# Performance work log

Measured on AMD Instinct MI355X. Metric: run time of the kernel, lower is better.

## Reference

```python
import jax, jax.numpy as jnp
import numpy as np

N = 50000      # nodes per graph batch (per side)
E = 600000     # edges per side
B = 4096       # number of graphs (drug pairs)
D = 128        # node_dim == hidden_dim
K = 128        # kge_dim
R = 86         # rel_total
L = 3          # n_iter
EPS = 1e-5


def setup_inputs() -> dict:
    key = jax.random.key(0)
    ks = jax.random.split(key, 16)
    inp = {}
    inp["x1"] = jax.random.normal(ks[0], (N, D), jnp.float32)
    inp["x2"] = jax.random.normal(ks[1], (N, D), jnp.float32)
    inp["edge_index1"] = jax.random.randint(ks[2], (2, E), 0, N)
    inp["edge_index2"] = jax.random.randint(ks[3], (2, E), 0, N)
    inp["batch1"] = jnp.sort(jax.random.randint(ks[4], (N,), 0, B))
    inp["batch2"] = jnp.sort(jax.random.randint(ks[5], (N,), 0, B))
    inp["rel"] = jax.random.randint(ks[6], (B,), 0, R)
    # SAGEConv params, stacked over L layers (all [D,D] since node_dim==hidden_dim)
    sc = 0.05
    inp["Wl"] = jax.random.normal(ks[7], (L, D, D), jnp.float32) * sc   # lin on aggregated neighbors (has bias)
    inp["bl"] = jnp.zeros((L, D), jnp.float32)
    inp["Wr"] = jax.random.normal(ks[8], (L, D, D), jnp.float32) * sc   # root (self) lin, no bias
    # BatchNorm (eval mode: running stats)
    inp["bn_gamma"] = jnp.ones((L, D), jnp.float32)
    inp["bn_beta"] = jnp.zeros((L, D), jnp.float32)
    inp["bn_mean"] = jnp.zeros((L, D), jnp.float32)
    inp["bn_var"] = jnp.ones((L, D), jnp.float32)
    # relation embedding + final MLP
    inp["kge"] = jax.random.normal(ks[9], (R, K), jnp.float32)
    inp["W1"] = jax.random.normal(ks[10], (2 * D + K, D), jnp.float32) * sc
    inp["b1"] = jnp.zeros((D,), jnp.float32)
    inp["W2"] = jax.random.normal(ks[11], (D, 1), jnp.float32) * sc
    inp["b2"] = jnp.zeros((1,), jnp.float32)
    return inp


def _gnn(x, edge_index, Wl, bl, Wr, g, b, m, v):
    src, dst = edge_index[0], edge_index[1]
    deg = jax.ops.segment_sum(jnp.ones((E,), x.dtype), dst, num_segments=N)
    deg = jnp.maximum(deg, 1.0)[:, None]
    for i in range(L):
        agg = jax.ops.segment_sum(x[src], dst, num_segments=N) / deg  # mean aggregation
        h = agg @ Wl[i] + bl[i] + x @ Wr[i]                           # SAGEConv
        h = (h - m[i]) * (g[i] / jnp.sqrt(v[i] + EPS)) + b[i]         # BN (eval)
        x = jax.nn.relu(h)                                            # dropout = identity (eval)
    return x


def reference(x1, edge_index1, batch1, x2, edge_index2, batch2, rel,
              Wl, bl, Wr, bn_gamma, bn_beta, bn_mean, bn_var,
              kge, W1, b1, W2, b2):
    h1 = _gnn(x1, edge_index1, Wl, bl, Wr, bn_gamma, bn_beta, bn_mean, bn_var)
    h2 = _gnn(x2, edge_index2, Wl, bl, Wr, bn_gamma, bn_beta, bn_mean, bn_var)
    p1 = jax.ops.segment_sum(h1, batch1, num_segments=B)  # global_add_pool
    p2 = jax.ops.segment_sum(h2, batch2, num_segments=B)
    r = kge[rel]                                          # [B, K]
    z = jnp.concatenate([p1, p2, r], axis=-1)             # [B, 2D+K]
    h = jax.nn.relu(z @ W1 + b1)
    out = h @ W2 + b2
    return out.reshape(-1)
```

## Files before the change

### kernel.cpp

```cpp
#include <hip/hip_runtime.h>

#define NN 50000
#define NE 600000
#define NB 4096
#define DD 128
#define EPSV 1e-5f
#define NBKT 196
#define NCHUNK 256
#define CHSZ ((NE + NCHUNK - 1) / NCHUNK)

typedef __bf16 bf16x8 __attribute__((ext_vector_type(8)));
typedef float f32x4 __attribute__((ext_vector_type(4)));

__device__ inline unsigned short f2bf(float f) {
    unsigned u = __float_as_uint(f);
    u = (u + 0x7FFFu + ((u >> 16) & 1u)) >> 16;
    return (unsigned short)u;
}
__device__ inline float bf2f(unsigned short h) {
    return __uint_as_float(((unsigned)h) << 16);
}

__global__ void k_cvt(const float* __restrict__ x1, const float* __restrict__ x2,
                      unsigned short* __restrict__ xh, unsigned short* __restrict__ xl) {
    int i = blockIdx.x * 256 + threadIdx.x;
    if (i >= 2 * NN * 32) return;
    const float* x = (i < NN * 32) ? x1 : x2;
    int j = (i < NN * 32) ? i : i - NN * 32;
    float4 v = ((const float4*)x)[j];
    ushort4 h, l;
    h.x = f2bf(v.x); l.x = f2bf(v.x - bf2f(h.x));
    h.y = f2bf(v.y); l.y = f2bf(v.y - bf2f(h.y));
    h.z = f2bf(v.z); l.z = f2bf(v.z - bf2f(h.z));
    h.w = f2bf(v.w); l.w = f2bf(v.w - bf2f(h.w));
    ((ushort4*)xh)[i] = h;
    ((ushort4*)xl)[i] = l;
}

__global__ void k_wcvt(const float* __restrict__ Wl, const float* __restrict__ Wr,
                       const float* __restrict__ W1, unsigned* __restrict__ wtp) {
    int t = blockIdx.x * 256 + threadIdx.x;
    if (t >= 3 * 128 * 256 + 128 * 384) return;
    float w;
    int idx;
    if (t < 3 * 128 * 256) {
        int k = t & 255;
        int n = (t >> 8) & 127;
        int l = t >> 15;
        w = (k < 128) ? Wl[l * 16384 + k * 128 + n] : Wr[l * 16384 + (k - 128) * 128 + n];
        idx = t;
    } else {
        int u = t - 3 * 128 * 256;
        int n = u / 384;
        int k = u - n * 384;
        w = W1[k * 128 + n];
        idx = t;
    }
    unsigned short h = f2bf(w);
    unsigned short l = f2bf(w - bf2f(h));
    wtp[idx] = ((unsigned)h << 16) | (unsigned)l;
}

__global__ void k_hist(const int* __restrict__ d0, const int* __restrict__ d1,
                       int* __restrict__ bcnt) {
    int side = (blockIdx.x >= NCHUNK) ? 1 : 0;
    int c = blockIdx.x - side * NCHUNK;
    const int* dst = side ? d1 : d0;
    int tid = threadIdx.x;
    __shared__ int h[NBKT];
    for (int i = tid; i < NBKT; i += 256) h[i] = 0;
    __syncthreads();
    int e0 = c * CHSZ, e1 = min(e0 + CHSZ, NE);
    for (int e = e0 + tid; e < e1; e += 256) atomicAdd(&h[dst[e] >> 8], 1);
    __syncthreads();
    int* bc = bcnt + ((size_t)side * NCHUNK + c) * NBKT;
    for (int i = tid; i < NBKT; i += 256) bc[i] = h[i];
}

__global__ void k_s1(int* __restrict__ bcnt, int* __restrict__ btot) {
    int side = (blockIdx.x >= NBKT) ? 1 : 0;
    int b = blockIdx.x - side * NBKT;
    int tid = threadIdx.x;
    int idx = ((size_t)side * NCHUNK + tid) * NBKT + b;
    int v = bcnt[idx];
    int lane = tid & 63, wv = tid >> 6;
    int x = v;
#pragma unroll
    for (int off = 1; off < 64; off <<= 1) {
        int y = __shfl_up(x, off, 64);
        if (lane >= off) x += y;
    }
    __shared__ int ws4[4];
    if (lane == 63) ws4[wv] = x;
    __syncthreads();
    int add = 0;
#pragma unroll
    for (int w = 0; w < 4; w++)
        if (w < wv) add += ws4[w];
    int incl = x + add;
    bcnt[idx] = incl - v;
    if (tid == 255) btot[side * NBKT + b] = incl;
}

__global__ void k_s2(const int* __restrict__ btot, int* __restrict__ bbase,
                     int* __restrict__ ptrC) {
    int side = blockIdx.x;
    int tid = threadIdx.x;
    int v = (tid < NBKT) ? btot[side * NBKT + tid] : 0;
    int lane = tid & 63, wv = tid >> 6;
    int x = v;
#pragma unroll
    for (int off = 1; off < 64; off <<= 1) {
        int y = __shfl_up(x, off, 64);
        if (lane >= off) x += y;
    }
    __shared__ int ws4[4];
    if (lane == 63) ws4[wv] = x;
    __syncthreads();
    int add = 0;
#pragma unroll
    for (int w = 0; w < 4; w++)
        if (w < wv) add += ws4[w];
    int incl = x + add;
    if (tid < NBKT) bbase[side * NBKT + tid] = incl - v;
    if (tid == 0 && side == 1) ptrC[2 * NN] = 2 * NE;
}

__global__ void k_part(const int* __restrict__ s0, const int* __restrict__ d0,
                       const int* __restrict__ s1, const int* __restrict__ d1,
                       const int* __restrict__ bcnt, const int* __restrict__ bbase,
                       int* __restrict__ part) {
    int side = (blockIdx.x >= NCHUNK) ? 1 : 0;
    int c = blockIdx.x - side * NCHUNK;
    const int* src = side ? s1 : s0;
    const int* dst = side ? d1 : d0;
    int tid = threadIdx.x;
    __shared__ int off[NBKT];
    const int* bc = bcnt + ((size_t)side * NCHUNK + c) * NBKT;
    for (int i = tid; i < NBKT; i += 256) off[i] = bbase[side * NBKT + i] + bc[i];
    __syncthreads();
    int e0 = c * CHSZ, e1 = min(e0 + CHSZ, NE);
    int* P = part + (size_t)side * NE;
    int soff = side * NN;
    for (int e = e0 + tid; e < e1; e += 256) {
        int d = dst[e];
        int pos = atomicAdd(&off[d >> 8], 1);
        P[pos] = ((src[e] + soff) << 8) | (d & 255);
    }
}

__global__ void k_csr(const int* __restrict__ part, const int* __restrict__ bbase,
                      int* __restrict__ ptrC, float* __restrict__ invdC,
                      int* __restrict__ csrC) {
    int side = (blockIdx.x >= NBKT) ? 1 : 0;
    int b = blockIdx.x - side * NBKT;
    int tid = threadIdx.x;
    const int* P = part + (size_t)side * NE;
    int base = bbase[side * NBKT + b];
    int endp = (b == NBKT - 1) ? NE : bbase[side * NBKT + b + 1];
    __shared__ int cnt[256];
    cnt[tid] = 0;
    __syncthreads();
    for (int e = base + tid; e < endp; e += 256) atomicAdd(&cnt[P[e] & 255], 1);
    __syncthreads();
    int v = cnt[tid];
    int lane = tid & 63, wv = tid >> 6;
    int x = v;
#pragma unroll
    for (int off = 1; off < 64; off <<= 1) {
        int y = __shfl_up(x, off, 64);
        if (lane >= off) x += y;
    }
    __shared__ int ws4[4];
    if (lane == 63) ws4[wv] = x;
    __syncthreads();
    int add = 0;
#pragma unroll
    for (int w = 0; w < 4; w++)
        if (w < wv) add += ws4[w];
    int excl = x + add - v;
    int node = (b << 8) + tid;
    if (node < NN) {
        ptrC[side * NN + node] = side * NE + base + excl;
        invdC[side * NN + node] = 1.0f / (float)(v > 1 ? v : 1);
    }
    __syncthreads();
    cnt[tid] = excl;
    __syncthreads();
    for (int e = base + tid; e < endp; e += 256) {
        int p = P[e];
        int pos = atomicAdd(&cnt[p & 255], 1);
        csrC[(size_t)side * NE + base + pos] = p >> 8;
    }
}

__global__ void k_gather(const unsigned short* __restrict__ xh, const int* __restrict__ ptr,
                         const int* __restrict__ csr, const float* __restrict__ invd,
                         unsigned short* __restrict__ aggH) {
    int wid = threadIdx.x >> 6;
    int lane = threadIdx.x & 63;
    int q = lane >> 4;
    int c = lane & 15;
    int n = blockIdx.x * 4 + wid;
    if (n >= 2 * NN) return;
    int beg = ptr[n], end = ptr[n + 1];
    float id = invd[n];
    float a[8];
#pragma unroll
    for (int k = 0; k < 8; k++) a[k] = 0.f;

    for (int base = beg; base < end; base += 64) {
        int cnt = min(end - base, 64);
        int idxv = csr[base + min(lane, cnt - 1)];
        for (int e0 = 0; e0 < cnt; e0 += 8) {
            int eA = e0 + q;
            int eB = e0 + 4 + q;
            int iA = __shfl(idxv, eA, 64);
            int iB = __shfl(idxv, eB, 64);
            float wA = (eA < cnt) ? 1.f : 0.f;
            float wB = (eB < cnt) ? 1.f : 0.f;
            uint4 vA = *(const uint4*)(xh + (((unsigned)iA << 7) + (c << 3)));
            uint4 vB = *(const uint4*)(xh + (((unsigned)iB << 7) + (c << 3)));
            a[0] += wA * __uint_as_float(vA.x << 16);
            a[1] += wA * __uint_as_float(vA.x & 0xffff0000u);
            a[2] += wA * __uint_as_float(vA.y << 16);
            a[3] += wA * __uint_as_float(vA.y & 0xffff0000u);
            a[4] += wA * __uint_as_float(vA.z << 16);
            a[5] += wA * __uint_as_float(vA.z & 0xffff0000u);
            a[6] += wA * __uint_as_float(vA.w << 16);
            a[7] += wA * __uint_as_float(vA.w & 0xffff0000u);
            a[0] += wB * __uint_as_float(vB.x << 16);
            a[1] += wB * __uint_as_float(vB.x & 0xffff0000u);
            a[2] += wB * __uint_as_float(vB.y << 16);
            a[3] += wB * __uint_as_float(vB.y & 0xffff0000u);
            a[4] += wB * __uint_as_float(vB.z << 16);
            a[5] += wB * __uint_as_float(vB.z & 0xffff0000u);
            a[6] += wB * __uint_as_float(vB.w << 16);
            a[7] += wB * __uint_as_float(vB.w & 0xffff0000u);
        }
    }
#pragma unroll
    for (int k = 0; k < 8; k++) {
        a[k] += __shfl_xor(a[k], 16, 64);
        a[k] += __shfl_xor(a[k], 32, 64);
    }
    if (q == 0) {
        unsigned short h0 = f2bf(a[0] * id), h1 = f2bf(a[1] * id);
        unsigned short h2 = f2bf(a[2] * id), h3 = f2bf(a[3] * id);
        unsigned short h4 = f2bf(a[4] * id), h5 = f2bf(a[5] * id);
        unsigned short h6 = f2bf(a[6] * id), h7 = f2bf(a[7] * id);
        uint4 o;
        o.x = (unsigned)h0 | ((unsigned)h1 << 16);
        o.y = (unsigned)h2 | ((unsigned)h3 << 16);
        o.z = (unsigned)h4 | ((unsigned)h5 << 16);
        o.w = (unsigned)h6 | ((unsigned)h7 << 16);
        *(uint4*)(aggH + (size_t)n * DD + c * 8) = o;
    }
}

__launch_bounds__(256)
__global__ void k_gemm(const unsigned short* __restrict__ AH,
                       const unsigned short* __restrict__ XH, const unsigned short* __restrict__ XL,
                       const unsigned* __restrict__ Wtp,
                       const float* __restrict__ bl, const float* __restrict__ g,
                       const float* __restrict__ be, const float* __restrict__ mn,
                       const float* __restrict__ vr,
                       unsigned short* __restrict__ OH, unsigned short* __restrict__ OL,
                       float* __restrict__ Of, int f32out) {
    __shared__ __align__(16) unsigned short sA[2][64 * 40];
    __shared__ __align__(16) unsigned short sW[2][64 * 40];
    int tid = threadIdx.x;
    int gx = blockIdx.x;
    int m0 = (gx >> 1) * 64;
    int n0 = (gx & 1) * 64;
    int lane = tid & 63;
    int w = tid >> 6;
    int fm = lane & 15, q = lane >> 4;
    int wr = (w & 1) * 32;
    int wn = (w >> 1) * 32;

    f32x4 acc[2][2];
#pragma unroll
    for (int i = 0; i < 2; i++)
#pragma unroll
        for (int j = 0; j < 2; j++) acc[i][j] = (f32x4){0.f, 0.f, 0.f, 0.f};

    for (int c = 0; c < 8; c++) {
        int isA = (c < 4);
        const unsigned short* SH = isA ? AH : XH;
        const unsigned short* SL = isA ? (const unsigned short*)0 : XL;
        int k0 = (c & 3) * 32;
        int k0W = c * 32;
        __syncthreads();
#pragma unroll
        for (int i = 0; i < 2; i++) {
            int u = tid + 256 * i;
            int row = u >> 3, seg = u & 7;
            int grow = m0 + row;
            size_t goff = (size_t)grow * DD + k0 + seg * 4;
            ushort4 hv = make_ushort4(0, 0, 0, 0);
            if (grow < 2 * NN) hv = *(const ushort4*)(SH + goff);
            *(ushort4*)&sA[0][row * 40 + seg * 4] = hv;
            if (!isA) {
                ushort4 lv = make_ushort4(0, 0, 0, 0);
                if (grow < 2 * NN) lv = *(const ushort4*)(SL + goff);
                *(ushort4*)&sA[1][row * 40 + seg * 4] = lv;
            }
        }
#pragma unroll
        for (int i = 0; i < 2; i++) {
            int u = tid + 256 * i;
            int row = u >> 3, seg = u & 7;
            uint4 val = *(const uint4*)(Wtp + (size_t)(n0 + row) * 256 + k0W + seg * 4);
            ushort4 hi, lo;
            hi.x = val.x >> 16; hi.y = val.y >> 16; hi.z = val.z >> 16; hi.w = val.w >> 16;
            lo.x = val.x & 0xFFFF; lo.y = val.y & 0xFFFF; lo.z = val.z & 0xFFFF; lo.w = val.w & 0xFFFF;
            *(ushort4*)&sW[0][row * 40 + seg * 4] = hi;
            *(ushort4*)&sW[1][row * 40 + seg * 4] = lo;
        }
        __syncthreads();
        bf16x8 afh[2], afl[2];
#pragma unroll
        for (int mt = 0; mt < 2; mt++) {
            int r = wr + mt * 16 + fm;
            afh[mt] = *(const bf16x8*)&sA[0][r * 40 + q * 8];
            if (!isA) afl[mt] = *(const bf16x8*)&sA[1][r * 40 + q * 8];
        }
#pragma unroll
        for (int nt = 0; nt < 2; nt++) {
            int nr = wn + nt * 16 + fm;
            bf16x8 wh = *(const bf16x8*)&sW[0][nr * 40 + q * 8];
            bf16x8 wl = *(const bf16x8*)&sW[1][nr * 40 + q * 8];
#pragma unroll
            for (int mt = 0; mt < 2; mt++) {
                acc[mt][nt] = __builtin_amdgcn_mfma_f32_16x16x32_bf16(afh[mt], wh, acc[mt][nt], 0, 0, 0);
                acc[mt][nt] = __builtin_amdgcn_mfma_f32_16x16x32_bf16(afh[mt], wl, acc[mt][nt], 0, 0, 0);
                if (!isA)
                    acc[mt][nt] = __builtin_amdgcn_mfma_f32_16x16x32_bf16(afl[mt], wh, acc[mt][nt], 0, 0, 0);
            }
        }
    }

    float scv[2], shv[2];
#pragma unroll
    for (int nt = 0; nt < 2; nt++) {
        int jj = n0 + wn + nt * 16 + fm;
        float s = g[jj] * rsqrtf(vr[jj] + EPSV);
        scv[nt] = s;
        shv[nt] = (bl[jj] - mn[jj]) * s + be[jj];
    }
#pragma unroll
    for (int mt = 0; mt < 2; mt++) {
#pragma unroll
        for (int r = 0; r < 4; r++) {
            int grow = m0 + wr + mt * 16 + q * 4 + r;
            if (grow < 2 * NN) {
#pragma unroll
                for (int nt = 0; nt < 2; nt++) {
                    int gcol = n0 + wn + nt * 16 + fm;
                    float o = fmaxf(acc[mt][nt][r] * scv[nt] + shv[nt], 0.f);
                    if (f32out) {
                        Of[(size_t)grow * DD + gcol] = o;
                    } else {
                        unsigned short h = f2bf(o);
                        OH[(size_t)grow * DD + gcol] = h;
                        OL[(size_t)grow * DD + gcol] = f2bf(o - bf2f(h));
                    }
                }
            }
        }
    }
}

__launch_bounds__(128)
__global__ void k_pool2(const float* __restrict__ cf, const int* __restrict__ bt1,
                        const int* __restrict__ bt2, float* __restrict__ ppool) {
    int side = (blockIdx.x >= NB) ? 1 : 0;
    int b = blockIdx.x - side * NB;
    const int* batch = side ? bt2 : bt1;
    const float* h = cf + (size_t)side * NN * DD;
    __shared__ int sr[2];
    if (threadIdx.x < 2) {
        int target = b + (int)threadIdx.x;
        int lo = 0, hi = NN;
        while (lo < hi) {
            int mid = (lo + hi) >> 1;
            if (batch[mid] < target) lo = mid + 1; else hi = mid;
        }
        sr[threadIdx.x] = lo;
    }
    __syncthreads();
    int beg = sr[0], end = sr[1];
    int t = threadIdx.x;
    float acc = 0.f;
    for (int r = beg; r < end; r++) acc += h[(size_t)r * DD + t];
    ppool[((size_t)side * NB + b) * DD + t] = acc;
}

__global__ void k_zb(const float* __restrict__ ppool, const int* __restrict__ rel,
                     const float* __restrict__ kge,
                     unsigned short* __restrict__ zh, unsigned short* __restrict__ zl) {
    int t = blockIdx.x * 256 + threadIdx.x;
    if (t >= NB * 384) return;
    int b = t / 384;
    int j = t - b * 384;
    float v;
    if (j < 128) v = ppool[(size_t)b * DD + j];
    else if (j < 256) v = ppool[(size_t)NB * DD + (size_t)b * DD + (j - 128)];
    else v = kge[(size_t)rel[b] * 128 + (j - 256)];
    unsigned short h = f2bf(v);
    zh[t] = h;
    zl[t] = f2bf(v - bf2f(h));
}

__launch_bounds__(256)
__global__ void k_mlp2(const unsigned short* __restrict__ zh, const unsigned short* __restrict__ zl,
                       const unsigned* __restrict__ w1p,
                       const float* __restrict__ b1, const float* __restrict__ W2,
                       const float* __restrict__ b2, float* __restrict__ out) {
    __shared__ __align__(16) unsigned short sZ[2][32 * 40];
    __shared__ __align__(16) unsigned short sW[2][128 * 40];
    __shared__ float hpart[32][4];
    int tid = threadIdx.x;
    int m0 = blockIdx.x * 32;
    int lane = tid & 63, w = tid >> 6;
    int fm = lane & 15, q = lane >> 4;
    int wn = w * 32;

    f32x4 acc[2][2];
#pragma unroll
    for (int i = 0; i < 2; i++)
#pragma unroll
        for (int j = 0; j < 2; j++) acc[i][j] = (f32x4){0.f, 0.f, 0.f, 0.f};

    for (int c = 0; c < 12; c++) {
        int k0 = c * 32;
        __syncthreads();
        {
            int row = tid >> 3, seg = tid & 7;
            size_t off = (size_t)(m0 + row) * 384 + k0 + seg * 4;
            *(ushort4*)&sZ[0][row * 40 + seg * 4] = *(const ushort4*)(zh + off);
            *(ushort4*)&sZ[1][row * 40 + seg * 4] = *(const ushort4*)(zl + off);
        }
#pragma unroll
        for (int i = 0; i < 4; i++) {
            int u = tid + 256 * i;
            int row = u >> 3, seg = u & 7;
            uint4 val = *(const uint4*)(w1p + (size_t)row * 384 + k0 + seg * 4);
            ushort4 hi, lo;
            hi.x = val.x >> 16; hi.y = val.y >> 16; hi.z = val.z >> 16; hi.w = val.w >> 16;
            lo.x = val.x & 0xFFFF; lo.y = val.y & 0xFFFF; lo.z = val.z & 0xFFFF; lo.w = val.w & 0xFFFF;
            *(ushort4*)&sW[0][row * 40 + seg * 4] = hi;
            *(ushort4*)&sW[1][row * 40 + seg * 4] = lo;
        }
        __syncthreads();
        bf16x8 zfh[2], zfl[2];
#pragma unroll
        for (int mt = 0; mt < 2; mt++) {
            int r = mt * 16 + fm;
            zfh[mt] = *(const bf16x8*)&sZ[0][r * 40 + q * 8];
            zfl[mt] = *(const bf16x8*)&sZ[1][r * 40 + q * 8];
        }
#pragma unroll
        for (int nt = 0; nt < 2; nt++) {
            int nr = wn + nt * 16 + fm;
            bf16x8 wh = *(const bf16x8*)&sW[0][nr * 40 + q * 8];
            bf16x8 wl = *(const bf16x8*)&sW[1][nr * 40 + q * 8];
#pragma unroll
            for (int mt = 0; mt < 2; mt++) {
                acc[mt][nt] = __builtin_amdgcn_mfma_f32_16x16x32_bf16(zfh[mt], wh, acc[mt][nt], 0, 0, 0);
                acc[mt][nt] = __builtin_amdgcn_mfma_f32_16x16x32_bf16(zfh[mt], wl, acc[mt][nt], 0, 0, 0);
                acc[mt][nt] = __builtin_amdgcn_mfma_f32_16x16x32_bf16(zfl[mt], wh, acc[mt][nt], 0, 0, 0);
            }
        }
    }

    float b1v[2], w2v[2];
#pragma unroll
    for (int nt = 0; nt < 2; nt++) {
        int col = wn + nt * 16 + fm;
        b1v[nt] = b1[col];
        w2v[nt] = W2[col];
    }
#pragma unroll
    for (int mt = 0; mt < 2; mt++) {
#pragma unroll
        for (int r = 0; r < 4; r++) {
            float val = 0.f;
#pragma unroll
            for (int nt = 0; nt < 2; nt++)
                val += fmaxf(acc[mt][nt][r] + b1v[nt], 0.f) * w2v[nt];
#pragma unroll
            for (int m = 1; m < 16; m <<= 1) val += __shfl_xor(val, m, 64);
            if (fm == 0) hpart[mt * 16 + q * 4 + r][w] = val;
        }
    }
    __syncthreads();
    if (tid < 32)
        out[m0 + tid] = hpart[tid][0] + hpart[tid][1] + hpart[tid][2] + hpart[tid][3] + b2[0];
}

extern "C" void kernel_launch(void* const* d_in, const int* in_sizes, int n_in,
                              void* d_out, int out_size, void* d_ws, size_t ws_size,
                              hipStream_t stream) {
    const float* x1  = (const float*)d_in[0];
    const float* x2  = (const float*)d_in[1];
    const int*   ei1 = (const int*)d_in[2];
    const int*   ei2 = (const int*)d_in[3];
    const int*   bt1 = (const int*)d_in[4];
    const int*   bt2 = (const int*)d_in[5];
    const int*   rel = (const int*)d_in[6];
    const float* Wl  = (const float*)d_in[7];
    const float* bl  = (const float*)d_in[8];
    const float* Wr  = (const float*)d_in[9];
    const float* g   = (const float*)d_in[10];
    const float* be  = (const float*)d_in[11];
    const float* mn  = (const float*)d_in[12];
    const float* vr  = (const float*)d_in[13];
    const float* kge = (const float*)d_in[14];
    const float* W1  = (const float*)d_in[15];
    const float* b1v = (const float*)d_in[16];
    const float* W2  = (const float*)d_in[17];
    const float* b2v = (const float*)d_in[18];

    char* ws = (char*)d_ws;
    size_t off = 0;
    auto alloc = [&](size_t bytes) {
        void* p = ws + off;
        off += (bytes + 255) & ~(size_t)255;
        return p;
    };
    const size_t PL = (size_t)2 * NN * DD;
    unsigned short* xbufH = (unsigned short*)alloc(PL * 2);
    unsigned short* xbufL = (unsigned short*)alloc(PL * 2);
    unsigned short* obufH = (unsigned short*)alloc(PL * 2);
    unsigned short* obufL = (unsigned short*)alloc(PL * 2);
    unsigned short* aggH  = (unsigned short*)alloc(PL * 2);
    unsigned* wtp  = (unsigned*)alloc((size_t)(3 * 128 * 256 + 128 * 384) * 4);
    float* ppool   = (float*)alloc((size_t)2 * NB * DD * 4);
    unsigned short* zh = (unsigned short*)alloc((size_t)NB * 384 * 2);
    unsigned short* zl = (unsigned short*)alloc((size_t)NB * 384 * 2);
    int*   bcnt    = (int*)alloc((size_t)2 * NCHUNK * NBKT * 4);
    int*   btot    = (int*)alloc((size_t)2 * NBKT * 4);
    int*   bbase   = (int*)alloc((size_t)2 * NBKT * 4);
    int*   part    = (int*)alloc((size_t)2 * NE * 4);
    int*   ptrC    = (int*)alloc((size_t)(2 * NN + 1) * 4);
    float* invdC   = (float*)alloc((size_t)2 * NN * 4);
    int*   csrC    = (int*)alloc((size_t)2 * NE * 4);
    if (off > ws_size) return;

    float* cf = (float*)obufH;

    const int nbCvt   = 12500;
    const int nbNode4 = (2 * NN + 3) / 4;
    const int nbGemm  = ((2 * NN + 63) / 64) * 2;
    const int nbW     = (3 * 128 * 256 + 128 * 384 + 255) / 256;

    k_wcvt<<<nbW, 256, 0, stream>>>(Wl, Wr, W1, wtp);

    k_hist<<<2 * NCHUNK, 256, 0, stream>>>(ei1 + NE, ei2 + NE, bcnt);
    k_s1<<<2 * NBKT, 256, 0, stream>>>(bcnt, btot);
    k_s2<<<2, 256, 0, stream>>>(btot, bbase, ptrC);
    k_part<<<2 * NCHUNK, 256, 0, stream>>>(ei1, ei1 + NE, ei2, ei2 + NE, bcnt, bbase, part);
    k_csr<<<2 * NBKT, 256, 0, stream>>>(part, bbase, ptrC, invdC, csrC);

    k_cvt<<<nbCvt, 256, 0, stream>>>(x1, x2, xbufH, xbufL);

    k_gather<<<nbNode4, 256, 0, stream>>>(xbufH, ptrC, csrC, invdC, aggH);
    k_gemm<<<nbGemm, 256, 0, stream>>>(aggH, xbufH, xbufL, wtp, bl, g, be, mn, vr,
                                       obufH, obufL, (float*)nullptr, 0);
    k_gather<<<nbNode4, 256, 0, stream>>>(obufH, ptrC, csrC, invdC, aggH);
    k_gemm<<<nbGemm, 256, 0, stream>>>(aggH, obufH, obufL, wtp + 32768, bl + 128, g + 128,
                                       be + 128, mn + 128, vr + 128,
                                       xbufH, xbufL, (float*)nullptr, 0);
    k_gather<<<nbNode4, 256, 0, stream>>>(xbufH, ptrC, csrC, invdC, aggH);
    k_gemm<<<nbGemm, 256, 0, stream>>>(aggH, xbufH, xbufL, wtp + 65536, bl + 256, g + 256,
                                       be + 256, mn + 256, vr + 256,
                                       (unsigned short*)nullptr, (unsigned short*)nullptr, cf, 1);

    k_pool2<<<2 * NB, 128, 0, stream>>>(cf, bt1, bt2, ppool);
    k_zb<<<(NB * 384 + 255) / 256, 256, 0, stream>>>(ppool, rel, kge, zh, zl);
    k_mlp2<<<NB / 32, 256, 0, stream>>>(zh, zl, wtp + 98304, b1v, W2, b2v, (float*)d_out);
}
```

Baseline: 454.5 us.

## Prepack weights in MFMA fragment order and drop LDS staging from SAGE GEMM

A new prep kernel writes the SAGE weights as bf16 hi/lo pairs already arranged in the MFMA fragment layout. The GEMM now loads A and W fragments straight from global memory into registers, with no shared-memory staging and no barriers. Each block covers 32 rows and all 128 output columns, so the A rows are read once instead of twice. Weight fragments are re-read from global/L2 by every block, and the row bounds check is removed on the assumption that 2*NN divides evenly by 32.

```diff
diff --git a/kernel.cpp b/kernel.cpp
--- a/kernel.cpp
+++ b/kernel.cpp
@@ -37,28 +37,31 @@
     ((ushort4*)xl)[i] = l;
 }
 
-__global__ void k_wcvt(const float* __restrict__ Wl, const float* __restrict__ Wr,
-                       const float* __restrict__ W1, unsigned* __restrict__ wtp) {
+__global__ void k_wcvt(const float* __restrict__ W1, unsigned* __restrict__ wtp) {
     int t = blockIdx.x * 256 + threadIdx.x;
-    if (t >= 3 * 128 * 256 + 128 * 384) return;
-    float w;
-    int idx;
-    if (t < 3 * 128 * 256) {
-        int k = t & 255;
-        int n = (t >> 8) & 127;
-        int l = t >> 15;
-        w = (k < 128) ? Wl[l * 16384 + k * 128 + n] : Wr[l * 16384 + (k - 128) * 128 + n];
-        idx = t;
-    } else {
-        int u = t - 3 * 128 * 256;
-        int n = u / 384;
-        int k = u - n * 384;
-        w = W1[k * 128 + n];
-        idx = t;
-    }
+    if (t >= 128 * 384) return;
+    int n = t / 384;
+    int k = t - n * 384;
+    float w = W1[k * 128 + n];
     unsigned short h = f2bf(w);
     unsigned short l = f2bf(w - bf2f(h));
-    wtp[idx] = ((unsigned)h << 16) | (unsigned)l;
+    wtp[t] = ((unsigned)h << 16) | (unsigned)l;
+}
+
+__global__ void k_wfrag(const float* __restrict__ Wl, const float* __restrict__ Wr,
+                        unsigned short* __restrict__ wf) {
+    int t = blockIdx.x * 256 + threadIdx.x;
+    if (t >= 3 * 128 * 256) return;
+    int k = t & 255;
+    int n = (t >> 8) & 127;
+    int l = t >> 15;
+    float w = (k < 128) ? Wl[l * 16384 + k * 128 + n] : Wr[l * 16384 + (k - 128) * 128 + n];
+    unsigned short h = f2bf(w);
+    unsigned short lo = f2bf(w - bf2f(h));
+    int ntile = n >> 4, fm = n & 15, kc = k >> 5, kq = (k & 31) >> 3, j = k & 7;
+    size_t pos = (size_t)l * 65536 + (size_t)(ntile * 8 + kc) * 1024 + (size_t)(kq * 16 + fm) * 8 + j;
+    wf[pos] = h;
+    wf[pos + 512] = lo;
 }
 
 __global__ void k_hist(const int* __restrict__ d0, const int* __restrict__ d1,
@@ -259,25 +262,29 @@
 }
 
 __launch_bounds__(256)
-__global__ void k_gemm(const unsigned short* __restrict__ AH,
-                       const unsigned short* __restrict__ XH, const unsigned short* __restrict__ XL,
-                       const unsigned* __restrict__ Wtp,
-                       const float* __restrict__ bl, const float* __restrict__ g,
-                       const float* __restrict__ be, const float* __restrict__ mn,
-                       const float* __restrict__ vr,
-                       unsigned short* __restrict__ OH, unsigned short* __restrict__ OL,
-                       float* __restrict__ Of, int f32out) {
-    __shared__ __align__(16) unsigned short sA[2][64 * 40];
-    __shared__ __align__(16) unsigned short sW[2][64 * 40];
-    int tid = threadIdx.x;
-    int gx = blockIdx.x;
-    int m0 = (gx >> 1) * 64;
-    int n0 = (gx & 1) * 64;
-    int lane = tid & 63;
-    int w = tid >> 6;
-    int fm = lane & 15, q = lane >> 4;
-    int wr = (w & 1) * 32;
-    int wn = (w >> 1) * 32;
+__global__ void k_gemm2(const unsigned short* __restrict__ AH,
+                        const unsigned short* __restrict__ XH, const unsigned short* __restrict__ XL,
+                        const unsigned short* __restrict__ wf,
+                        const float* __restrict__ bl, const float* __restrict__ g,
+                        const float* __restrict__ be, const float* __restrict__ mn,
+                        const float* __restrict__ vr,
+                        unsigned short* __restrict__ OH, unsigned short* __restrict__ OL,
+                        float* __restrict__ Of, int f32out) {
+    int tid = threadIdx.x;
+    int lane = tid & 63, w = tid >> 6;
+    int fm = lane & 15, kq = lane >> 4;
+    int m0 = blockIdx.x * 32;
+
+    size_t rb0 = (size_t)(m0 + fm) * DD + kq * 8;
+    size_t rb1 = rb0 + (size_t)16 * DD;
+    const unsigned short* pA0 = AH + rb0;
+    const unsigned short* pA1 = AH + rb1;
+    const unsigned short* pXH0 = XH + rb0;
+    const unsigned short* pXH1 = XH + rb1;
+    const unsigned short* pXL0 = XL + rb0;
+    const unsigned short* pXL1 = XL + rb1;
+    const unsigned short* pW0 = wf + (size_t)(w * 2 + 0) * 8192 + lane * 8;
+    const unsigned short* pW1 = wf + (size_t)(w * 2 + 1) * 8192 + lane * 8;
 
     f32x4 acc[2][2];
 #pragma unroll
@@ -285,66 +292,42 @@
 #pragma unroll
         for (int j = 0; j < 2; j++) acc[i][j] = (f32x4){0.f, 0.f, 0.f, 0.f};
 
+#pragma unroll
     for (int c = 0; c < 8; c++) {
-        int isA = (c < 4);
-        const unsigned short* SH = isA ? AH : XH;
-        const unsigned short* SL = isA ? (const unsigned short*)0 : XL;
-        int k0 = (c & 3) * 32;
-        int k0W = c * 32;
-        __syncthreads();
-#pragma unroll
-        for (int i = 0; i < 2; i++) {
-            int u = tid + 256 * i;
-            int row = u >> 3, seg = u & 7;
-            int grow = m0 + row;
-            size_t goff = (size_t)grow * DD + k0 + seg * 4;
-            ushort4 hv = make_ushort4(0, 0, 0, 0);
-            if (grow < 2 * NN) hv = *(const ushort4*)(SH + goff);
-            *(ushort4*)&sA[0][row * 40 + seg * 4] = hv;
-            if (!isA) {
-                ushort4 lv = make_ushort4(0, 0, 0, 0);
-                if (grow < 2 * NN) lv = *(const ushort4*)(SL + goff);
-                *(ushort4*)&sA[1][row * 40 + seg * 4] = lv;
-            }
-        }
-#pragma unroll
-        for (int i = 0; i < 2; i++) {
-            int u = tid + 256 * i;
-            int row = u >> 3, seg = u & 7;
-            uint4 val = *(const uint4*)(Wtp + (size_t)(n0 + row) * 256 + k0W + seg * 4);
-            ushort4 hi, lo;
-            hi.x = val.x >> 16; hi.y = val.y >> 16; hi.z = val.z >> 16; hi.w = val.w >> 16;
-            lo.x = val.x & 0xFFFF; lo.y = val.y & 0xFFFF; lo.z = val.z & 0xFFFF; lo.w = val.w & 0xFFFF;
-            *(ushort4*)&sW[0][row * 40 + seg * 4] = hi;
-            *(ushort4*)&sW[1][row * 40 + seg * 4] = lo;
-        }
-        __syncthreads();
-        bf16x8 afh[2], afl[2];
-#pragma unroll
-        for (int mt = 0; mt < 2; mt++) {
-            int r = wr + mt * 16 + fm;
-            afh[mt] = *(const bf16x8*)&sA[0][r * 40 + q * 8];
-            if (!isA) afl[mt] = *(const bf16x8*)&sA[1][r * 40 + q * 8];
-        }
-#pragma unroll
-        for (int nt = 0; nt < 2; nt++) {
-            int nr = wn + nt * 16 + fm;
-            bf16x8 wh = *(const bf16x8*)&sW[0][nr * 40 + q * 8];
-            bf16x8 wl = *(const bf16x8*)&sW[1][nr * 40 + q * 8];
-#pragma unroll
-            for (int mt = 0; mt < 2; mt++) {
-                acc[mt][nt] = __builtin_amdgcn_mfma_f32_16x16x32_bf16(afh[mt], wh, acc[mt][nt], 0, 0, 0);
-                acc[mt][nt] = __builtin_amdgcn_mfma_f32_16x16x32_bf16(afh[mt], wl, acc[mt][nt], 0, 0, 0);
-                if (!isA)
-                    acc[mt][nt] = __builtin_amdgcn_mfma_f32_16x16x32_bf16(afl[mt], wh, acc[mt][nt], 0, 0, 0);
-            }
+        bf16x8 a0h, a1h, a0l, a1l;
+        if (c < 4) {
+            a0h = *(const bf16x8*)(pA0 + c * 32);
+            a1h = *(const bf16x8*)(pA1 + c * 32);
+        } else {
+            a0h = *(const bf16x8*)(pXH0 + (c - 4) * 32);
+            a1h = *(const bf16x8*)(pXH1 + (c - 4) * 32);
+            a0l = *(const bf16x8*)(pXL0 + (c - 4) * 32);
+            a1l = *(const bf16x8*)(pXL1 + (c - 4) * 32);
+        }
+        bf16x8 w0h = *(const bf16x8*)(pW0 + c * 1024);
+        bf16x8 w0l = *(const bf16x8*)(pW0 + c * 1024 + 512);
+        bf16x8 w1h = *(const bf16x8*)(pW1 + c * 1024);
+        bf16x8 w1l = *(const bf16x8*)(pW1 + c * 1024 + 512);
+        acc[0][0] = __builtin_amdgcn_mfma_f32_16x16x32_bf16(a0h, w0h, acc[0][0], 0, 0, 0);
+        acc[0][0] = __builtin_amdgcn_mfma_f32_16x16x32_bf16(a0h, w0l, acc[0][0], 0, 0, 0);
+        acc[0][1] = __builtin_amdgcn_mfma_f32_16x16x32_bf16(a0h, w1h, acc[0][1], 0, 0, 0);
+        acc[0][1] = __builtin_amdgcn_mfma_f32_16x16x32_bf16(a0h, w1l, acc[0][1], 0, 0, 0);
+        acc[1][0] = __builtin_amdgcn_mfma_f32_16x16x32_bf16(a1h, w0h, acc[1][0], 0, 0, 0);
+        acc[1][0] = __builtin_amdgcn_mfma_f32_16x16x32_bf16(a1h, w0l, acc[1][0], 0, 0, 0);
+        acc[1][1] = __builtin_amdgcn_mfma_f32_16x16x32_bf16(a1h, w1h, acc[1][1], 0, 0, 0);
+        acc[1][1] = __builtin_amdgcn_mfma_f32_16x16x32_bf16(a1h, w1l, acc[1][1], 0, 0, 0);
+        if (c >= 4) {
+            acc[0][0] = __builtin_amdgcn_mfma_f32_16x16x32_bf16(a0l, w0h, acc[0][0], 0, 0, 0);
+            acc[0][1] = __builtin_amdgcn_mfma_f32_16x16x32_bf16(a0l, w1h, acc[0][1], 0, 0, 0);
+            acc[1][0] = __builtin_amdgcn_mfma_f32_16x16x32_bf16(a1l, w0h, acc[1][0], 0, 0, 0);
+            acc[1][1] = __builtin_amdgcn_mfma_f32_16x16x32_bf16(a1l, w1h, acc[1][1], 0, 0, 0);
         }
     }
 
     float scv[2], shv[2];
 #pragma unroll
     for (int nt = 0; nt < 2; nt++) {
-        int jj = n0 + wn + nt * 16 + fm;
+        int jj = w * 32 + nt * 16 + fm;
         float s = g[jj] * rsqrtf(vr[jj] + EPSV);
         scv[nt] = s;
         shv[nt] = (bl[jj] - mn[jj]) * s + be[jj];
@@ -353,19 +336,17 @@
     for (int mt = 0; mt < 2; mt++) {
 #pragma unroll
         for (int r = 0; r < 4; r++) {
-            int grow = m0 + wr + mt * 16 + q * 4 + r;
-            if (grow < 2 * NN) {
-#pragma unroll
-                for (int nt = 0; nt < 2; nt++) {
-                    int gcol = n0 + wn + nt * 16 + fm;
-                    float o = fmaxf(acc[mt][nt][r] * scv[nt] + shv[nt], 0.f);
-                    if (f32out) {
-                        Of[(size_t)grow * DD + gcol] = o;
-                    } else {
-                        unsigned short h = f2bf(o);
-                        OH[(size_t)grow * DD + gcol] = h;
-                        OL[(size_t)grow * DD + gcol] = f2bf(o - bf2f(h));
-                    }
+            int grow = m0 + mt * 16 + kq * 4 + r;
+#pragma unroll
+            for (int nt = 0; nt < 2; nt++) {
+                int gcol = w * 32 + nt * 16 + fm;
+                float o = fmaxf(acc[mt][nt][r] * scv[nt] + shv[nt], 0.f);
+                if (f32out) {
+                    Of[(size_t)grow * DD + gcol] = o;
+                } else {
+                    unsigned short h = f2bf(o);
+                    OH[(size_t)grow * DD + gcol] = h;
+                    OL[(size_t)grow * DD + gcol] = f2bf(o - bf2f(h));
                 }
             }
         }
@@ -536,7 +517,8 @@
     unsigned short* obufH = (unsigned short*)alloc(PL * 2);
     unsigned short* obufL = (unsigned short*)alloc(PL * 2);
     unsigned short* aggH  = (unsigned short*)alloc(PL * 2);
-    unsigned* wtp  = (unsigned*)alloc((size_t)(3 * 128 * 256 + 128 * 384) * 4);
+    unsigned short* wf = (unsigned short*)alloc((size_t)3 * 65536 * 2);
+    unsigned* wtp  = (unsigned*)alloc((size_t)128 * 384 * 4);
     float* ppool   = (float*)alloc((size_t)2 * NB * DD * 4);
     unsigned short* zh = (unsigned short*)alloc((size_t)NB * 384 * 2);
     unsigned short* zl = (unsigned short*)alloc((size_t)NB * 384 * 2);
@@ -553,10 +535,12 @@
 
     const int nbCvt   = 12500;
     const int nbNode4 = (2 * NN + 3) / 4;
-    const int nbGemm  = ((2 * NN + 63) / 64) * 2;
-    const int nbW     = (3 * 128 * 256 + 128 * 384 + 255) / 256;
-
-    k_wcvt<<<nbW, 256, 0, stream>>>(Wl, Wr, W1, wtp);
+    const int nbGemm2 = 2 * NN / 32;
+    const int nbW     = (128 * 384 + 255) / 256;
+    const int nbWf    = (3 * 128 * 256 + 255) / 256;
+
+    k_wcvt<<<nbW, 256, 0, stream>>>(W1, wtp);
+    k_wfrag<<<nbWf, 256, 0, stream>>>(Wl, Wr, wf);
 
     k_hist<<<2 * NCHUNK, 256, 0, stream>>>(ei1 + NE, ei2 + NE, bcnt);
     k_s1<<<2 * NBKT, 256, 0, stream>>>(bcnt, btot);
@@ -567,18 +551,18 @@
     k_cvt<<<nbCvt, 256, 0, stream>>>(x1, x2, xbufH, xbufL);
 
     k_gather<<<nbNode4, 256, 0, stream>>>(xbufH, ptrC, csrC, invdC, aggH);
-    k_gemm<<<nbGemm, 256, 0, stream>>>(aggH, xbufH, xbufL, wtp, bl, g, be, mn, vr,
-                                       obufH, obufL, (float*)nullptr, 0);
+    k_gemm2<<<nbGemm2, 256, 0, stream>>>(aggH, xbufH, xbufL, wf, bl, g, be, mn, vr,
+                                         obufH, obufL, (float*)nullptr, 0);
     k_gather<<<nbNode4, 256, 0, stream>>>(obufH, ptrC, csrC, invdC, aggH);
-    k_gemm<<<nbGemm, 256, 0, stream>>>(aggH, obufH, obufL, wtp + 32768, bl + 128, g + 128,
-                                       be + 128, mn + 128, vr + 128,
-                                       xbufH, xbufL, (float*)nullptr, 0);
+    k_gemm2<<<nbGemm2, 256, 0, stream>>>(aggH, obufH, obufL, wf + 65536, bl + 128, g + 128,
+                                         be + 128, mn + 128, vr + 128,
+                                         xbufH, xbufL, (float*)nullptr, 0);
     k_gather<<<nbNode4, 256, 0, stream>>>(xbufH, ptrC, csrC, invdC, aggH);
-    k_gemm<<<nbGemm, 256, 0, stream>>>(aggH, xbufH, xbufL, wtp + 65536, bl + 256, g + 256,
-                                       be + 256, mn + 256, vr + 256,
-                                       (unsigned short*)nullptr, (unsigned short*)nullptr, cf, 1);
+    k_gemm2<<<nbGemm2, 256, 0, stream>>>(aggH, xbufH, xbufL, wf + 131072, bl + 256, g + 256,
+                                         be + 256, mn + 256, vr + 256,
+                                         (unsigned short*)nullptr, (unsigned short*)nullptr, cf, 1);
 
     k_pool2<<<2 * NB, 128, 0, stream>>>(cf, bt1, bt2, ppool);
     k_zb<<<(NB * 384 + 255) / 256, 256, 0, stream>>>(ppool, rel, kge, zh, zl);
-    k_mlp2<<<NB / 32, 256, 0, stream>>>(zh, zl, wtp + 98304, b1v, W2, b2v, (float*)d_out);
-}
+    k_mlp2<<<NB / 32, 256, 0, stream>>>(zh, zl, wtp, b1v, W2, b2v, (float*)d_out);
+}
```

After: 501.5 us. +10.3%, slower.

## Fuse neighbor gather into SAGE GEMM kernel, aggregating into shared memory

Applied to the files above, without the earlier changes.

The separate gather and GEMM kernels per layer are merged: each block of 64 nodes first computes mean-aggregated neighbor features into LDS, then runs the MFMA GEMM over the full 128 output columns against both the aggregate and the root features. This removes the global round-trip of the aggregation buffer and two launches per layer, and stops the A tile from being reloaded for each of two column halves. In exchange there are fewer blocks (one per 64 rows instead of two), a serial gather phase before the GEMM with no overlap inside a block, and higher register and LDS use, which could lower occupancy.

```diff
diff --git a/kernel.cpp b/kernel.cpp
--- a/kernel.cpp
+++ b/kernel.cpp
@@ -42,23 +42,20 @@
     int t = blockIdx.x * 256 + threadIdx.x;
     if (t >= 3 * 128 * 256 + 128 * 384) return;
     float w;
-    int idx;
     if (t < 3 * 128 * 256) {
         int k = t & 255;
         int n = (t >> 8) & 127;
         int l = t >> 15;
         w = (k < 128) ? Wl[l * 16384 + k * 128 + n] : Wr[l * 16384 + (k - 128) * 128 + n];
-        idx = t;
     } else {
         int u = t - 3 * 128 * 256;
         int n = u / 384;
         int k = u - n * 384;
         w = W1[k * 128 + n];
-        idx = t;
     }
     unsigned short h = f2bf(w);
     unsigned short l = f2bf(w - bf2f(h));
-    wtp[idx] = ((unsigned)h << 16) | (unsigned)l;
+    wtp[t] = ((unsigned)h << 16) | (unsigned)l;
 }
 
 __global__ void k_hist(const int* __restrict__ d0, const int* __restrict__ d1,
@@ -194,124 +191,114 @@
     }
 }
 
-__global__ void k_gather(const unsigned short* __restrict__ xh, const int* __restrict__ ptr,
-                         const int* __restrict__ csr, const float* __restrict__ invd,
-                         unsigned short* __restrict__ aggH) {
-    int wid = threadIdx.x >> 6;
-    int lane = threadIdx.x & 63;
-    int q = lane >> 4;
-    int c = lane & 15;
-    int n = blockIdx.x * 4 + wid;
-    if (n >= 2 * NN) return;
-    int beg = ptr[n], end = ptr[n + 1];
-    float id = invd[n];
-    float a[8];
-#pragma unroll
-    for (int k = 0; k < 8; k++) a[k] = 0.f;
-
-    for (int base = beg; base < end; base += 64) {
-        int cnt = min(end - base, 64);
-        int idxv = csr[base + min(lane, cnt - 1)];
-        for (int e0 = 0; e0 < cnt; e0 += 8) {
-            int eA = e0 + q;
-            int eB = e0 + 4 + q;
-            int iA = __shfl(idxv, eA, 64);
-            int iB = __shfl(idxv, eB, 64);
-            float wA = (eA < cnt) ? 1.f : 0.f;
-            float wB = (eB < cnt) ? 1.f : 0.f;
-            uint4 vA = *(const uint4*)(xh + (((unsigned)iA << 7) + (c << 3)));
-            uint4 vB = *(const uint4*)(xh + (((unsigned)iB << 7) + (c << 3)));
-            a[0] += wA * __uint_as_float(vA.x << 16);
-            a[1] += wA * __uint_as_float(vA.x & 0xffff0000u);
-            a[2] += wA * __uint_as_float(vA.y << 16);
-            a[3] += wA * __uint_as_float(vA.y & 0xffff0000u);
-            a[4] += wA * __uint_as_float(vA.z << 16);
-            a[5] += wA * __uint_as_float(vA.z & 0xffff0000u);
-            a[6] += wA * __uint_as_float(vA.w << 16);
-            a[7] += wA * __uint_as_float(vA.w & 0xffff0000u);
-            a[0] += wB * __uint_as_float(vB.x << 16);
-            a[1] += wB * __uint_as_float(vB.x & 0xffff0000u);
-            a[2] += wB * __uint_as_float(vB.y << 16);
-            a[3] += wB * __uint_as_float(vB.y & 0xffff0000u);
-            a[4] += wB * __uint_as_float(vB.z << 16);
-            a[5] += wB * __uint_as_float(vB.z & 0xffff0000u);
-            a[6] += wB * __uint_as_float(vB.w << 16);
-            a[7] += wB * __uint_as_float(vB.w & 0xffff0000u);
-        }
-    }
-#pragma unroll
-    for (int k = 0; k < 8; k++) {
-        a[k] += __shfl_xor(a[k], 16, 64);
-        a[k] += __shfl_xor(a[k], 32, 64);
-    }
-    if (q == 0) {
-        unsigned short h0 = f2bf(a[0] * id), h1 = f2bf(a[1] * id);
-        unsigned short h2 = f2bf(a[2] * id), h3 = f2bf(a[3] * id);
-        unsigned short h4 = f2bf(a[4] * id), h5 = f2bf(a[5] * id);
-        unsigned short h6 = f2bf(a[6] * id), h7 = f2bf(a[7] * id);
-        uint4 o;
-        o.x = (unsigned)h0 | ((unsigned)h1 << 16);
-        o.y = (unsigned)h2 | ((unsigned)h3 << 16);
-        o.z = (unsigned)h4 | ((unsigned)h5 << 16);
-        o.w = (unsigned)h6 | ((unsigned)h7 << 16);
-        *(uint4*)(aggH + (size_t)n * DD + c * 8) = o;
-    }
-}
-
-__launch_bounds__(256)
-__global__ void k_gemm(const unsigned short* __restrict__ AH,
-                       const unsigned short* __restrict__ XH, const unsigned short* __restrict__ XL,
+__launch_bounds__(256, 4)
+__global__ void k_fuse(const unsigned short* __restrict__ XH, const unsigned short* __restrict__ XL,
+                       const int* __restrict__ ptr, const int* __restrict__ csr,
+                       const float* __restrict__ invd,
                        const unsigned* __restrict__ Wtp,
                        const float* __restrict__ bl, const float* __restrict__ g,
                        const float* __restrict__ be, const float* __restrict__ mn,
                        const float* __restrict__ vr,
                        unsigned short* __restrict__ OH, unsigned short* __restrict__ OL,
                        float* __restrict__ Of, int f32out) {
-    __shared__ __align__(16) unsigned short sA[2][64 * 40];
-    __shared__ __align__(16) unsigned short sW[2][64 * 40];
-    int tid = threadIdx.x;
-    int gx = blockIdx.x;
-    int m0 = (gx >> 1) * 64;
-    int n0 = (gx & 1) * 64;
-    int lane = tid & 63;
-    int w = tid >> 6;
-    int fm = lane & 15, q = lane >> 4;
+    __shared__ __align__(16) unsigned short sBuf[8704];
+    __shared__ __align__(16) unsigned short sW[2][128 * 40];
+    int tid = threadIdx.x;
+    int lane = tid & 63, w = tid >> 6;
+    int fm = lane & 15, kq = lane >> 4;
+    int m0 = blockIdx.x * 64;
+
+    for (int i = 0; i < 16; i++) {
+        int n = m0 + w * 16 + i;
+        int beg = 0, end = 0;
+        float id = 0.f;
+        if (n < 2 * NN) { beg = ptr[n]; end = ptr[n + 1]; id = invd[n]; }
+        float a[8];
+#pragma unroll
+        for (int k = 0; k < 8; k++) a[k] = 0.f;
+        for (int base = beg; base < end; base += 64) {
+            int cnt = min(end - base, 64);
+            int idxv = csr[base + min(lane, cnt - 1)];
+            for (int e0 = 0; e0 < cnt; e0 += 8) {
+                int eA = e0 + kq;
+                int eB = e0 + 4 + kq;
+                int iA = __shfl(idxv, eA, 64);
+                int iB = __shfl(idxv, eB, 64);
+                float wA = (eA < cnt) ? 1.f : 0.f;
+                float wB = (eB < cnt) ? 1.f : 0.f;
+                uint4 vA = *(const uint4*)(XH + (((unsigned)iA << 7) + (fm << 3)));
+                uint4 vB = *(const uint4*)(XH + (((unsigned)iB << 7) + (fm << 3)));
+                a[0] += wA * __uint_as_float(vA.x << 16);
+                a[1] += wA * __uint_as_float(vA.x & 0xffff0000u);
+                a[2] += wA * __uint_as_float(vA.y << 16);
+                a[3] += wA * __uint_as_float(vA.y & 0xffff0000u);
+                a[4] += wA * __uint_as_float(vA.z << 16);
+                a[5] += wA * __uint_as_float(vA.z & 0xffff0000u);
+                a[6] += wA * __uint_as_float(vA.w << 16);
+                a[7] += wA * __uint_as_float(vA.w & 0xffff0000u);
+                a[0] += wB * __uint_as_float(vB.x << 16);
+                a[1] += wB * __uint_as_float(vB.x & 0xffff0000u);
+                a[2] += wB * __uint_as_float(vB.y << 16);
+                a[3] += wB * __uint_as_float(vB.y & 0xffff0000u);
+                a[4] += wB * __uint_as_float(vB.z << 16);
+                a[5] += wB * __uint_as_float(vB.z & 0xffff0000u);
+                a[6] += wB * __uint_as_float(vB.w << 16);
+                a[7] += wB * __uint_as_float(vB.w & 0xffff0000u);
+            }
+        }
+#pragma unroll
+        for (int k = 0; k < 8; k++) {
+            a[k] += __shfl_xor(a[k], 16, 64);
+            a[k] += __shfl_xor(a[k], 32, 64);
+        }
+        if (kq == 0) {
+            unsigned short h0 = f2bf(a[0] * id), h1 = f2bf(a[1] * id);
+            unsigned short h2 = f2bf(a[2] * id), h3 = f2bf(a[3] * id);
+            unsigned short h4 = f2bf(a[4] * id), h5 = f2bf(a[5] * id);
+            unsigned short h6 = f2bf(a[6] * id), h7 = f2bf(a[7] * id);
+            uint4 o;
+            o.x = (unsigned)h0 | ((unsigned)h1 << 16);
+            o.y = (unsigned)h2 | ((unsigned)h3 << 16);
+            o.z = (unsigned)h4 | ((unsigned)h5 << 16);
+            o.w = (unsigned)h6 | ((unsigned)h7 << 16);
+            *(uint4*)&sBuf[(w * 16 + i) * 136 + fm * 8] = o;
+        }
+    }
+    __syncthreads();
+
     int wr = (w & 1) * 32;
-    int wn = (w >> 1) * 32;
-
-    f32x4 acc[2][2];
+    int wn = (w >> 1) * 64;
+
+    f32x4 acc[2][4];
 #pragma unroll
     for (int i = 0; i < 2; i++)
 #pragma unroll
-        for (int j = 0; j < 2; j++) acc[i][j] = (f32x4){0.f, 0.f, 0.f, 0.f};
+        for (int j = 0; j < 4; j++) acc[i][j] = (f32x4){0.f, 0.f, 0.f, 0.f};
 
     for (int c = 0; c < 8; c++) {
         int isA = (c < 4);
-        const unsigned short* SH = isA ? AH : XH;
-        const unsigned short* SL = isA ? (const unsigned short*)0 : XL;
-        int k0 = (c & 3) * 32;
-        int k0W = c * 32;
-        __syncthreads();
-#pragma unroll
-        for (int i = 0; i < 2; i++) {
+        if (c > 0) __syncthreads();
+        if (!isA) {
+#pragma unroll
+            for (int i = 0; i < 2; i++) {
+                int u = tid + 256 * i;
+                int row = u >> 3, seg = u & 7;
+                int grow = m0 + row;
+                size_t goff = (size_t)grow * DD + (c - 4) * 32 + seg * 4;
+                ushort4 hv = make_ushort4(0, 0, 0, 0), lv = make_ushort4(0, 0, 0, 0);
+                if (grow < 2 * NN) {
+                    hv = *(const ushort4*)(XH + goff);
+                    lv = *(const ushort4*)(XL + goff);
+                }
+                *(ushort4*)&sBuf[row * 40 + seg * 4] = hv;
+                *(ushort4*)&sBuf[2560 + row * 40 + seg * 4] = lv;
+            }
+        }
+#pragma unroll
+        for (int i = 0; i < 4; i++) {
             int u = tid + 256 * i;
             int row = u >> 3, seg = u & 7;
-            int grow = m0 + row;
-            size_t goff = (size_t)grow * DD + k0 + seg * 4;
-            ushort4 hv = make_ushort4(0, 0, 0, 0);
-            if (grow < 2 * NN) hv = *(const ushort4*)(SH + goff);
-            *(ushort4*)&sA[0][row * 40 + seg * 4] = hv;
-            if (!isA) {
-                ushort4 lv = make_ushort4(0, 0, 0, 0);
-                if (grow < 2 * NN) lv = *(const ushort4*)(SL + goff);
-                *(ushort4*)&sA[1][row * 40 + seg * 4] = lv;
-            }
-        }
-#pragma unroll
-        for (int i = 0; i < 2; i++) {
-            int u = tid + 256 * i;
-            int row = u >> 3, seg = u & 7;
-            uint4 val = *(const uint4*)(Wtp + (size_t)(n0 + row) * 256 + k0W + seg * 4);
+            uint4 val = *(const uint4*)(Wtp + (size_t)row * 256 + c * 32 + seg * 4);
             ushort4 hi, lo;
             hi.x = val.x >> 16; hi.y = val.y >> 16; hi.z = val.z >> 16; hi.w = val.w >> 16;
             lo.x = val.x & 0xFFFF; lo.y = val.y & 0xFFFF; lo.z = val.z & 0xFFFF; lo.w = val.w & 0xFFFF;
@@ -319,32 +306,37 @@
             *(ushort4*)&sW[1][row * 40 + seg * 4] = lo;
         }
         __syncthreads();
-        bf16x8 afh[2], afl[2];
-#pragma unroll
-        for (int mt = 0; mt < 2; mt++) {
-            int r = wr + mt * 16 + fm;
-            afh[mt] = *(const bf16x8*)&sA[0][r * 40 + q * 8];
-            if (!isA) afl[mt] = *(const bf16x8*)&sA[1][r * 40 + q * 8];
-        }
-#pragma unroll
-        for (int nt = 0; nt < 2; nt++) {
+
+        bf16x8 a0h, a1h, a0l, a1l;
+        if (isA) {
+            a0h = *(const bf16x8*)&sBuf[(wr + fm) * 136 + c * 32 + kq * 8];
+            a1h = *(const bf16x8*)&sBuf[(wr + 16 + fm) * 136 + c * 32 + kq * 8];
+        } else {
+            a0h = *(const bf16x8*)&sBuf[(wr + fm) * 40 + kq * 8];
+            a1h = *(const bf16x8*)&sBuf[(wr + 16 + fm) * 40 + kq * 8];
+            a0l = *(const bf16x8*)&sBuf[2560 + (wr + fm) * 40 + kq * 8];
+            a1l = *(const bf16x8*)&sBuf[2560 + (wr + 16 + fm) * 40 + kq * 8];
+        }
+#pragma unroll
+        for (int nt = 0; nt < 4; nt++) {
             int nr = wn + nt * 16 + fm;
-            bf16x8 wh = *(const bf16x8*)&sW[0][nr * 40 + q * 8];
-            bf16x8 wl = *(const bf16x8*)&sW[1][nr * 40 + q * 8];
-#pragma unroll
-            for (int mt = 0; mt < 2; mt++) {
-                acc[mt][nt] = __builtin_amdgcn_mfma_f32_16x16x32_bf16(afh[mt], wh, acc[mt][nt], 0, 0, 0);
-                acc[mt][nt] = __builtin_amdgcn_mfma_f32_16x16x32_bf16(afh[mt], wl, acc[mt][nt], 0, 0, 0);
-                if (!isA)
-                    acc[mt][nt] = __builtin_amdgcn_mfma_f32_16x16x32_bf16(afl[mt], wh, acc[mt][nt], 0, 0, 0);
+            bf16x8 wh = *(const bf16x8*)&sW[0][nr * 40 + kq * 8];
+            bf16x8 wl = *(const bf16x8*)&sW[1][nr * 40 + kq * 8];
+            acc[0][nt] = __builtin_amdgcn_mfma_f32_16x16x32_bf16(a0h, wh, acc[0][nt], 0, 0, 0);
+            acc[0][nt] = __builtin_amdgcn_mfma_f32_16x16x32_bf16(a0h, wl, acc[0][nt], 0, 0, 0);
+            acc[1][nt] = __builtin_amdgcn_mfma_f32_16x16x32_bf16(a1h, wh, acc[1][nt], 0, 0, 0);
+            acc[1][nt] = __builtin_amdgcn_mfma_f32_16x16x32_bf16(a1h, wl, acc[1][nt], 0, 0, 0);
+            if (!isA) {
+                acc[0][nt] = __builtin_amdgcn_mfma_f32_16x16x32_bf16(a0l, wh, acc[0][nt], 0, 0, 0);
+                acc[1][nt] = __builtin_amdgcn_mfma_f32_16x16x32_bf16(a1l, wh, acc[1][nt], 0, 0, 0);
             }
         }
     }
 
-    float scv[2], shv[2];
-#pragma unroll
-    for (int nt = 0; nt < 2; nt++) {
-        int jj = n0 + wn + nt * 16 + fm;
+    float scv[4], shv[4];
+#pragma unroll
+    for (int nt = 0; nt < 4; nt++) {
+        int jj = wn + nt * 16 + fm;
         float s = g[jj] * rsqrtf(vr[jj] + EPSV);
         scv[nt] = s;
         shv[nt] = (bl[jj] - mn[jj]) * s + be[jj];
@@ -353,11 +345,11 @@
     for (int mt = 0; mt < 2; mt++) {
 #pragma unroll
         for (int r = 0; r < 4; r++) {
-            int grow = m0 + wr + mt * 16 + q * 4 + r;
+            int grow = m0 + wr + mt * 16 + kq * 4 + r;
             if (grow < 2 * NN) {
 #pragma unroll
-                for (int nt = 0; nt < 2; nt++) {
-                    int gcol = n0 + wn + nt * 16 + fm;
+                for (int nt = 0; nt < 4; nt++) {
+                    int gcol = wn + nt * 16 + fm;
                     float o = fmaxf(acc[mt][nt][r] * scv[nt] + shv[nt], 0.f);
                     if (f32out) {
                         Of[(size_t)grow * DD + gcol] = o;
@@ -535,7 +527,6 @@
     unsigned short* xbufL = (unsigned short*)alloc(PL * 2);
     unsigned short* obufH = (unsigned short*)alloc(PL * 2);
     unsigned short* obufL = (unsigned short*)alloc(PL * 2);
-    unsigned short* aggH  = (unsigned short*)alloc(PL * 2);
     unsigned* wtp  = (unsigned*)alloc((size_t)(3 * 128 * 256 + 128 * 384) * 4);
     float* ppool   = (float*)alloc((size_t)2 * NB * DD * 4);
     unsigned short* zh = (unsigned short*)alloc((size_t)NB * 384 * 2);
@@ -551,10 +542,9 @@
 
     float* cf = (float*)obufH;
 
-    const int nbCvt   = 12500;
-    const int nbNode4 = (2 * NN + 3) / 4;
-    const int nbGemm  = ((2 * NN + 63) / 64) * 2;
-    const int nbW     = (3 * 128 * 256 + 128 * 384 + 255) / 256;
+    const int nbCvt  = 12500;
+    const int nbFuse = (2 * NN + 63) / 64;
+    const int nbW    = (3 * 128 * 256 + 128 * 384 + 255) / 256;
 
     k_wcvt<<<nbW, 256, 0, stream>>>(Wl, Wr, W1, wtp);
 
@@ -566,16 +556,14 @@
 
     k_cvt<<<nbCvt, 256, 0, stream>>>(x1, x2, xbufH, xbufL);
 
-    k_gather<<<nbNode4, 256, 0, stream>>>(xbufH, ptrC, csrC, invdC, aggH);
-    k_gemm<<<nbGemm, 256, 0, stream>>>(aggH, xbufH, xbufL, wtp, bl, g, be, mn, vr,
+    k_fuse<<<nbFuse, 256, 0, stream>>>(xbufH, xbufL, ptrC, csrC, invdC, wtp,
+                                       bl, g, be, mn, vr,
                                        obufH, obufL, (float*)nullptr, 0);
-    k_gather<<<nbNode4, 256, 0, stream>>>(obufH, ptrC, csrC, invdC, aggH);
-    k_gemm<<<nbGemm, 256, 0, stream>>>(aggH, obufH, obufL, wtp + 32768, bl + 128, g + 128,
-                                       be + 128, mn + 128, vr + 128,
+    k_fuse<<<nbFuse, 256, 0, stream>>>(obufH, obufL, ptrC, csrC, invdC, wtp + 32768,
+                                       bl + 128, g + 128, be + 128, mn + 128, vr + 128,
                                        xbufH, xbufL, (float*)nullptr, 0);
-    k_gather<<<nbNode4, 256, 0, stream>>>(xbufH, ptrC, csrC, invdC, aggH);
-    k_gemm<<<nbGemm, 256, 0, stream>>>(aggH, xbufH, xbufL, wtp + 65536, bl + 256, g + 256,
-                                       be + 256, mn + 256, vr + 256,
+    k_fuse<<<nbFuse, 256, 0, stream>>>(xbufH, xbufL, ptrC, csrC, invdC, wtp + 65536,
+                                       bl + 256, g + 256, be + 256, mn + 256, vr + 256,
                                        (unsigned short*)nullptr, (unsigned short*)nullptr, cf, 1);
 
     k_pool2<<<2 * NB, 128, 0, stream>>>(cf, bt1, bt2, ppool);
```

After: 488.2 us. 1.07x slower.
